# Kernel optimization log

Hardware: AMD Instinct MI355X
Metric: run time of the kernel (lower is better)

Reference implementation:

```python
import jax, jax.numpy as jnp
import numpy as np

ATOM_F = 64
NBR_F = 41
EPS = 1e-05


def setup_inputs() -> dict:
    key = jax.random.key(0)
    ks = jax.random.split(key, 10)
    B, N, M = 512, 64, 12
    F, NF = ATOM_F, NBR_F
    atom_fea = jax.random.normal(ks[0], (B, N, F), dtype=jnp.float32)
    nbr_fea = jax.random.normal(ks[1], (B, N, M, NF), dtype=jnp.float32)
    nbr_fea_idx = jax.random.randint(ks[2], (B, N, M), 0, N, dtype=jnp.int32)
    mask = jax.random.randint(ks[3], (B, N, M, 2 * F), 0, 2, dtype=jnp.int32)
    lim = float(np.sqrt(6.0 / (2 * F + NF + 2 * F)))
    gc_W = jax.random.uniform(ks[4], (2 * F + NF, 2 * F), minval=-lim, maxval=lim, dtype=jnp.float32)
    gc_bias = jnp.zeros((2 * F,), jnp.float32)
    gamma_1 = jnp.ones((2 * F,), jnp.float32)
    beta_1 = jnp.zeros((2 * F,), jnp.float32)
    gamma_2 = jnp.ones((F,), jnp.float32)
    beta_2 = jnp.zeros((F,), jnp.float32)
    return {
        'atom_fea': atom_fea, 'nbr_fea': nbr_fea, 'gc_W': gc_W, 'gc_bias': gc_bias,
        'gamma_1': gamma_1, 'beta_1': beta_1, 'gamma_2': gamma_2, 'beta_2': beta_2,
        'nbr_fea_idx': nbr_fea_idx, 'mask': mask,
    }


def _bn(x, mu, var, gamma, beta):
    return (x - mu) * jax.lax.rsqrt(var + EPS) * gamma + beta


def reference(atom_fea, nbr_fea, gc_W, gc_bias, gamma_1, beta_1, gamma_2, beta_2, nbr_fea_idx, mask):
    B, N, M = nbr_fea_idx.shape
    F = atom_fea.shape[-1]
    m = mask.astype(jnp.float32)                       # [B,N,M,2F]
    # gather neighbor atom features per batch: [B,N,M,F]
    atom_nbr_fea = jax.vmap(lambda af, idx: af[idx])(atom_fea, nbr_fea_idx)
    atom_exp = jnp.broadcast_to(atom_fea[:, :, None, :], (B, N, M, F))
    total_nbr_fea = jnp.concatenate([atom_exp, atom_nbr_fea, nbr_fea], axis=3)
    total_gated = (jnp.einsum('bnmk,ko->bnmo', total_nbr_fea, gc_W) + gc_bias) * m
    # global masked batchnorm (scalar mu/var over all nonzero entries)
    cnt1 = jnp.count_nonzero(total_gated).astype(jnp.float32)
    mu_1 = jnp.sum(total_gated) / cnt1
    var_1 = jnp.sum((total_gated - mu_1) ** 2 * m) / cnt1
    total_gated = _bn(total_gated, mu_1, var_1, gamma_1, beta_1) * m
    nbr_filter, nbr_core = jnp.split(total_gated, 2, axis=3)
    gated = jax.nn.sigmoid(nbr_filter) * jax.nn.softplus(nbr_core)
    m_node = m[:, :, 0, :F]                            # [B,N,F]
    nbr_summed = jnp.sum(gated, axis=2) * m_node
    cnt2 = jnp.count_nonzero(nbr_summed).astype(jnp.float32)
    mu_2 = jnp.sum(nbr_summed) / cnt2
    diff2 = (nbr_summed - mu_2) ** 2 * m_node
    var_2 = jnp.sum(diff2) / jnp.count_nonzero(diff2).astype(jnp.float32)
    nbr_summed = _bn(nbr_summed, mu_2, var_2, gamma_2, beta_2) * m_node
    return jax.nn.softplus(atom_fea + nbr_summed) * m_node
```

## Files before the change

kernel.cpp:

```cpp
#include <hip/hip_runtime.h>
#include <hip/hip_bf16.h>

#define B_   512
#define N_   64
#define M_   12
#define F_   64
#define NF_  41
#define NODES (B_*N_)
#define ROWS  (NODES*M_)
#define GW    NODES
#define GBLK  (GW/4)
#define ABLK  1024
#define KTOT  169
#define CSTR  136

typedef __bf16 bf16x8 __attribute__((ext_vector_type(8)));
typedef float  f32x4  __attribute__((ext_vector_type(4)));
typedef float  f32x4u __attribute__((ext_vector_type(4), aligned(4)));

#define P1_OFF 1024
#define P2_OFF 525312
#define WF_OFF 537600
#define X_OFF  586752

__device__ __forceinline__ float waveReduce(float v) {
#pragma unroll
  for (int off = 32; off > 0; off >>= 1) v += __shfl_down(v, off, 64);
  return v;
}

__device__ __forceinline__ bf16x8 cvt8(f32x4 a, f32x4 b) {
  bf16x8 r;
  r[0] = (__bf16)a[0]; r[1] = (__bf16)a[1]; r[2] = (__bf16)a[2]; r[3] = (__bf16)a[3];
  r[4] = (__bf16)b[0]; r[5] = (__bf16)b[1]; r[6] = (__bf16)b[2]; r[7] = (__bf16)b[3];
  return r;
}

__global__ void k_wprep(const float* __restrict__ W, __bf16* __restrict__ Wf) {
  int t = blockIdx.x * 256 + threadIdx.x;
  if (t >= 6 * 8 * 64) return;
  int lane = t & 63, nt = (t >> 6) & 7, kc = t >> 9;
  int n  = nt * 16 + (lane & 15);
  int k0 = kc * 32 + (lane >> 4) * 8;
  bf16x8 v;
#pragma unroll
  for (int j = 0; j < 8; j++) {
    int k = k0 + j;
    v[j] = (k < KTOT) ? (__bf16)W[k * 128 + n] : (__bf16)0.f;
  }
  *reinterpret_cast<bf16x8*>(&Wf[(size_t)t * 8]) = v;
}

__global__ __launch_bounds__(256, 4) void k_gemm(
    const float* __restrict__ atom, const float* __restrict__ nbr,
    const int* __restrict__ idx, const int* __restrict__ mask,
    const __bf16* __restrict__ Wf, const float* __restrict__ bias,
    float* __restrict__ part1, __bf16* __restrict__ xout)
{
  __shared__ __bf16 Cs_all[4][12 * CSTR];

  const int tid  = threadIdx.x;
  const int w    = tid >> 6;
  const int lane = tid & 63;
  const int nlo  = lane & 15;
  const int quad = lane >> 4;
  const int g    = blockIdx.x * 4 + w;
  const int bb   = (g >> 6) << 6;
  __bf16* Cs = Cs_all[w];

  const int r  = (nlo < 11) ? nlo : 11;
  const int nb = idx[g * M_ + r];

  bf16x8 af[6];
  {
    const float* p = &atom[(size_t)g * F_ + quad * 8];
    f32x4 a0 = *(const f32x4*)p, b0 = *(const f32x4*)(p + 4);
    f32x4 a1 = *(const f32x4*)(p + 32), b1 = *(const f32x4*)(p + 36);
    af[0] = cvt8(a0, b0); af[1] = cvt8(a1, b1);
  }
  {
    const float* p = &atom[(size_t)(bb + nb) * F_ + quad * 8];
    f32x4 a0 = *(const f32x4*)p, b0 = *(const f32x4*)(p + 4);
    f32x4 a1 = *(const f32x4*)(p + 32), b1 = *(const f32x4*)(p + 36);
    af[2] = cvt8(a0, b0); af[3] = cvt8(a1, b1);
  }
  {
    const float* nrow = &nbr[(size_t)(g * M_ + r) * NF_];
    f32x4u a0 = *(const f32x4u*)(nrow + quad * 8);
    f32x4u b0 = *(const f32x4u*)(nrow + quad * 8 + 4);
    af[4] = cvt8((f32x4)a0, (f32x4)b0);
    float t[8];
#pragma unroll
    for (int j = 0; j < 8; j++) {
      int kp = 32 + quad * 8 + j;
      t[j] = (kp < NF_) ? nrow[kp] : 0.f;
    }
    bf16x8 v;
#pragma unroll
    for (int j = 0; j < 8; j++) v[j] = (__bf16)t[j];
    af[5] = v;
  }

  f32x4 acc[8];
#pragma unroll
  for (int nt = 0; nt < 8; nt++) acc[nt] = (f32x4){0.f, 0.f, 0.f, 0.f};

#pragma unroll
  for (int kc = 0; kc < 6; kc++) {
#pragma unroll
    for (int nt = 0; nt < 8; nt++) {
      bf16x8 bf = *reinterpret_cast<const bf16x8*>(
          &Wf[(size_t)(((kc * 8 + nt) * 64) + lane) * 8]);
      acc[nt] = __builtin_amdgcn_mfma_f32_16x16x32_bf16(af[kc], bf, acc[nt], 0, 0, 0);
    }
  }

  if (quad < 3) {
#pragma unroll
    for (int nt = 0; nt < 8; nt++) {
      float bv = bias[nt * 16 + nlo];
#pragma unroll
      for (int reg = 0; reg < 4; reg++) {
        int row = quad * 4 + reg;
        Cs[row * CSTR + nt * 16 + nlo] = (__bf16)(acc[nt][reg] + bv);
      }
    }
  }
  asm volatile("s_waitcnt lgkmcnt(0)" ::: "memory");

  float s = 0.f, ss = 0.f, cz = 0.f, cm = 0.f;
#pragma unroll
  for (int i = 0; i < 3; i++) {
    int ch = lane + i * 64;
    int row = ch >> 4, c = ch & 15;
    size_t grow = (size_t)g * M_ + row;
    bf16x8 yv = *reinterpret_cast<const bf16x8*>(&Cs[row * CSTR + c * 8]);
    const int4 mA = *(const int4*)&mask[grow * 128 + c * 8];
    const int4 mB = *(const int4*)&mask[grow * 128 + c * 8 + 4];
    int mv[8] = {mA.x, mA.y, mA.z, mA.w, mB.x, mB.y, mB.z, mB.w};
#pragma unroll
    for (int j = 0; j < 8; j++) {
      float y = (float)yv[j];
      if (!mv[j]) { y = 0.f; yv[j] = (__bf16)0.f; }
      s += y; ss += y * y;
      cz += (y != 0.f) ? 1.f : 0.f;
      cm += (float)mv[j];
    }
    *reinterpret_cast<bf16x8*>(&xout[grow * 128 + c * 8]) = yv;
  }

  float v0 = waveReduce(s), v1 = waveReduce(ss), v2 = waveReduce(cz), v3 = waveReduce(cm);
  if (lane == 0) {
    part1[0 * GW + g] = v0;
    part1[1 * GW + g] = v1;
    part1[2 * GW + g] = v2;
    part1[3 * GW + g] = v3;
  }
}

__global__ __launch_bounds__(256) void k_red1(const float* __restrict__ part1,
                                              float* __restrict__ scal) {
  __shared__ double red[256][4];
  int t = threadIdx.x;
  double a[4] = {0.0, 0.0, 0.0, 0.0};
  for (int i = t; i < GW; i += 256)
#pragma unroll
    for (int q = 0; q < 4; q++) a[q] += (double)part1[q * GW + i];
#pragma unroll
  for (int q = 0; q < 4; q++) red[t][q] = a[q];
  __syncthreads();
  for (int s = 128; s > 0; s >>= 1) {
    if (t < s)
#pragma unroll
      for (int q = 0; q < 4; q++) red[t][q] += red[t + s][q];
    __syncthreads();
  }
  if (t == 0) {
    double S = red[0][0], SS = red[0][1], CNZ = red[0][2], CM = red[0][3];
    double mu = 0.0, var = 0.0;
    if (CNZ > 0.5) {
      mu = S / CNZ;
      var = (SS - 2.0 * mu * S + mu * mu * CM) / CNZ;
    }
    scal[0] = (float)mu;
    scal[1] = (float)(1.0 / sqrt(var + 1e-5));
  }
}

__global__ __launch_bounds__(256) void k_act(
    const __bf16* __restrict__ x, const int* __restrict__ mask,
    const float* __restrict__ g1, const float* __restrict__ b1,
    const float* __restrict__ scal, float* __restrict__ part2,
    float* __restrict__ ns)
{
  __shared__ float red[3][4];
  int t = blockIdx.x * 256 + threadIdx.x;
  int g = t >> 3, o0 = (t & 7) * 8;

  float mu1 = scal[0], inv1 = scal[1];

  float kf[8], cf[8], kc[8], cc[8];
#pragma unroll
  for (int j = 0; j < 8; j++) {
    kf[j] = inv1 * g1[o0 + j];      cf[j] = b1[o0 + j]      - mu1 * kf[j];
    kc[j] = inv1 * g1[64 + o0 + j]; cc[j] = b1[64 + o0 + j] - mu1 * kc[j];
  }

  size_t base = (size_t)g * (M_ * 128) + o0;
  float ssum[8];
#pragma unroll
  for (int j = 0; j < 8; j++) ssum[j] = 0.f;

#pragma unroll
  for (int m = 0; m < M_; m++) {
    bf16x8 xf = *reinterpret_cast<const bf16x8*>(&x[base + m * 128]);
    bf16x8 xc = *reinterpret_cast<const bf16x8*>(&x[base + m * 128 + 64]);
#pragma unroll
    for (int j = 0; j < 8; j++) {
      float vf = (float)xf[j], vc = (float)xc[j];
      float yf = (vf != 0.f) ? fmaf(vf, kf[j], cf[j]) : 0.f;
      float yc = (vc != 0.f) ? fmaf(vc, kc[j], cc[j]) : 0.f;
      float sg = __builtin_amdgcn_rcpf(1.f + __expf(-yf));
      float sp = fmaxf(yc, 0.f) + __logf(1.f + __expf(-fabsf(yc)));
      ssum[j] += sg * sp;
    }
  }

  const int4 mA = *(const int4*)&mask[(size_t)g * (M_ * 128) + o0];
  const int4 mB = *(const int4*)&mask[(size_t)g * (M_ * 128) + o0 + 4];
  int mn[8] = {mA.x, mA.y, mA.z, mA.w, mB.x, mB.y, mB.z, mB.w};
  float s = 0.f, ss2 = 0.f, c = 0.f;
  float v[8];
#pragma unroll
  for (int j = 0; j < 8; j++) {
    v[j] = mn[j] ? ssum[j] : 0.f;
    s += v[j]; ss2 += v[j] * v[j];
    c += (v[j] != 0.f) ? 1.f : 0.f;
  }
  *(float4*)&ns[(size_t)g * 64 + o0]     = (float4){v[0], v[1], v[2], v[3]};
  *(float4*)&ns[(size_t)g * 64 + o0 + 4] = (float4){v[4], v[5], v[6], v[7]};

  float v0 = waveReduce(s), v1 = waveReduce(ss2), v2 = waveReduce(c);
  int lane = threadIdx.x & 63, wid = threadIdx.x >> 6;
  if (lane == 0) { red[0][wid] = v0; red[1][wid] = v1; red[2][wid] = v2; }
  __syncthreads();
  if (threadIdx.x < 3)
    part2[threadIdx.x * ABLK + blockIdx.x] =
        red[threadIdx.x][0] + red[threadIdx.x][1] + red[threadIdx.x][2] + red[threadIdx.x][3];
}

__global__ __launch_bounds__(256) void k_red2(const float* __restrict__ part2,
                                              float* __restrict__ scal) {
  __shared__ double red[256][3];
  int t = threadIdx.x;
  double a[3] = {0.0, 0.0, 0.0};
  for (int i = t; i < ABLK; i += 256)
#pragma unroll
    for (int q = 0; q < 3; q++) a[q] += (double)part2[q * ABLK + i];
#pragma unroll
  for (int q = 0; q < 3; q++) red[t][q] = a[q];
  __syncthreads();
  for (int s = 128; s > 0; s >>= 1) {
    if (t < s)
#pragma unroll
      for (int q = 0; q < 3; q++) red[t][q] += red[t + s][q];
    __syncthreads();
  }
  if (t == 0) {
    double S = red[0][0], SS = red[0][1], C = red[0][2];
    double mu = 0.0, var = 0.0;
    if (C > 0.5) {
      mu = S / C;
      var = (SS - 2.0 * mu * S + mu * mu * C) / C;
    }
    scal[2] = (float)mu;
    scal[3] = (float)(1.0 / sqrt(var + 1e-5));
  }
}

__global__ __launch_bounds__(256) void k_out(
    const float* __restrict__ atom, const float* __restrict__ ns,
    const float* __restrict__ g2, const float* __restrict__ b2,
    const float* __restrict__ scal, float* __restrict__ out)
{
  int t = blockIdx.x * 256 + threadIdx.x;
  int g = t >> 3, o0 = (t & 7) * 8;
  float mu2 = scal[2], inv2 = scal[3];

  float4 n0 = *(const float4*)&ns[(size_t)g * 64 + o0];
  float4 n1 = *(const float4*)&ns[(size_t)g * 64 + o0 + 4];
  float4 a0 = *(const float4*)&atom[(size_t)g * 64 + o0];
  float4 a1 = *(const float4*)&atom[(size_t)g * 64 + o0 + 4];
  float nv[8] = {n0.x, n0.y, n0.z, n0.w, n1.x, n1.y, n1.z, n1.w};
  float av[8] = {a0.x, a0.y, a0.z, a0.w, a1.x, a1.y, a1.z, a1.w};
  float r[8];
#pragma unroll
  for (int j = 0; j < 8; j++) {
    r[j] = 0.f;
    if (nv[j] != 0.f) {
      float bn = (nv[j] - mu2) * inv2 * g2[o0 + j] + b2[o0 + j];
      float a = av[j] + bn;
      r[j] = fmaxf(a, 0.f) + __logf(1.f + __expf(-fabsf(a)));
    }
  }
  *(float4*)&out[(size_t)g * 64 + o0]     = (float4){r[0], r[1], r[2], r[3]};
  *(float4*)&out[(size_t)g * 64 + o0 + 4] = (float4){r[4], r[5], r[6], r[7]};
}

extern "C" void kernel_launch(void* const* d_in, const int* in_sizes, int n_in,
                              void* d_out, int out_size, void* d_ws, size_t ws_size,
                              hipStream_t stream)
{
  const float* atom = (const float*)d_in[0];
  const float* nbr  = (const float*)d_in[1];
  const float* W    = (const float*)d_in[2];
  const float* bias = (const float*)d_in[3];
  const float* g1   = (const float*)d_in[4];
  const float* b1   = (const float*)d_in[5];
  const float* g2   = (const float*)d_in[6];
  const float* b2   = (const float*)d_in[7];
  const int*   idx  = (const int*)d_in[8];
  const int*   mask = (const int*)d_in[9];
  float* out = (float*)d_out;

  char* ws = (char*)d_ws;
  float*  scal  = (float*)ws;
  float*  part1 = (float*)(ws + P1_OFF);
  float*  part2 = (float*)(ws + P2_OFF);
  __bf16* Wf    = (__bf16*)(ws + WF_OFF);
  __bf16* x     = (__bf16*)(ws + X_OFF);
  float* ns = out;

  k_wprep<<<12, 256, 0, stream>>>(W, Wf);
  k_gemm<<<GBLK, 256, 0, stream>>>(atom, nbr, idx, mask, Wf, bias, part1, x);
  k_red1<<<1, 256, 0, stream>>>(part1, scal);
  k_act<<<(NODES * 8) / 256, 256, 0, stream>>>(x, mask, g1, b1, scal, part2, ns);
  k_red2<<<1, 256, 0, stream>>>(part2, scal);
  k_out<<<(NODES * 8) / 256, 256, 0, stream>>>(atom, ns, g2, b2, scal, out);
}
```

Measured before the change: 480.2 us.

## Retile gather-GEMM so waves split output columns and keep weights in registers

The GEMM kernel used to give each wave one node (12 rows, padded to 16) and all 128 output columns, reloading the full weight fragment set per wave. Now each block handles 4 nodes (48 rows, exactly three 16-row MFMA tiles) per iteration and loops over 8 groups. Each wave owns 32 output columns, so its weight fragments are loaded into registers once and reused across iterations. This removes the 25% padding waste and the repeated weight loads, but cuts block count by 8x, lowers the occupancy hint, and makes every wave redundantly gather the same A operands.

```diff
diff --git a/kernel.cpp b/kernel.cpp
--- a/kernel.cpp
+++ b/kernel.cpp
@@ -8,20 +8,22 @@
 #define NF_  41
 #define NODES (B_*N_)
 #define ROWS  (NODES*M_)
-#define GW    NODES
-#define GBLK  (GW/4)
+#define GRP   (NODES/4)
+#define ITER  8
+#define BLKS  (GRP/ITER)
+#define WSLOT (BLKS*4)
 #define ABLK  1024
 #define KTOT  169
-#define CSTR  136
+#define CSTR2 40
 
 typedef __bf16 bf16x8 __attribute__((ext_vector_type(8)));
 typedef float  f32x4  __attribute__((ext_vector_type(4)));
 typedef float  f32x4u __attribute__((ext_vector_type(4), aligned(4)));
 
 #define P1_OFF 1024
-#define P2_OFF 525312
-#define WF_OFF 537600
-#define X_OFF  586752
+#define P2_OFF 66560
+#define WF_OFF 78848
+#define X_OFF  128000
 
 __device__ __forceinline__ float waveReduce(float v) {
 #pragma unroll
@@ -51,110 +53,133 @@
   *reinterpret_cast<bf16x8*>(&Wf[(size_t)t * 8]) = v;
 }
 
-__global__ __launch_bounds__(256, 4) void k_gemm(
+__global__ __launch_bounds__(256, 3) void k_gemm(
     const float* __restrict__ atom, const float* __restrict__ nbr,
     const int* __restrict__ idx, const int* __restrict__ mask,
     const __bf16* __restrict__ Wf, const float* __restrict__ bias,
     float* __restrict__ part1, __bf16* __restrict__ xout)
 {
-  __shared__ __bf16 Cs_all[4][12 * CSTR];
+  __shared__ __bf16 Cs_all[4][48 * CSTR2];
 
   const int tid  = threadIdx.x;
   const int w    = tid >> 6;
   const int lane = tid & 63;
   const int nlo  = lane & 15;
   const int quad = lane >> 4;
-  const int g    = blockIdx.x * 4 + w;
-  const int bb   = (g >> 6) << 6;
   __bf16* Cs = Cs_all[w];
 
-  const int r  = (nlo < 11) ? nlo : 11;
-  const int nb = idx[g * M_ + r];
-
-  bf16x8 af[6];
-  {
-    const float* p = &atom[(size_t)g * F_ + quad * 8];
-    f32x4 a0 = *(const f32x4*)p, b0 = *(const f32x4*)(p + 4);
-    f32x4 a1 = *(const f32x4*)(p + 32), b1 = *(const f32x4*)(p + 36);
-    af[0] = cvt8(a0, b0); af[1] = cvt8(a1, b1);
-  }
-  {
-    const float* p = &atom[(size_t)(bb + nb) * F_ + quad * 8];
-    f32x4 a0 = *(const f32x4*)p, b0 = *(const f32x4*)(p + 4);
-    f32x4 a1 = *(const f32x4*)(p + 32), b1 = *(const f32x4*)(p + 36);
-    af[2] = cvt8(a0, b0); af[3] = cvt8(a1, b1);
-  }
-  {
-    const float* nrow = &nbr[(size_t)(g * M_ + r) * NF_];
-    f32x4u a0 = *(const f32x4u*)(nrow + quad * 8);
-    f32x4u b0 = *(const f32x4u*)(nrow + quad * 8 + 4);
-    af[4] = cvt8((f32x4)a0, (f32x4)b0);
-    float t[8];
-#pragma unroll
-    for (int j = 0; j < 8; j++) {
-      int kp = 32 + quad * 8 + j;
-      t[j] = (kp < NF_) ? nrow[kp] : 0.f;
-    }
-    bf16x8 v;
-#pragma unroll
-    for (int j = 0; j < 8; j++) v[j] = (__bf16)t[j];
-    af[5] = v;
-  }
-
-  f32x4 acc[8];
-#pragma unroll
-  for (int nt = 0; nt < 8; nt++) acc[nt] = (f32x4){0.f, 0.f, 0.f, 0.f};
-
-#pragma unroll
-  for (int kc = 0; kc < 6; kc++) {
-#pragma unroll
-    for (int nt = 0; nt < 8; nt++) {
-      bf16x8 bf = *reinterpret_cast<const bf16x8*>(
-          &Wf[(size_t)(((kc * 8 + nt) * 64) + lane) * 8]);
-      acc[nt] = __builtin_amdgcn_mfma_f32_16x16x32_bf16(af[kc], bf, acc[nt], 0, 0, 0);
-    }
-  }
-
-  if (quad < 3) {
-#pragma unroll
-    for (int nt = 0; nt < 8; nt++) {
-      float bv = bias[nt * 16 + nlo];
-#pragma unroll
-      for (int reg = 0; reg < 4; reg++) {
-        int row = quad * 4 + reg;
-        Cs[row * CSTR + nt * 16 + nlo] = (__bf16)(acc[nt][reg] + bv);
+  bf16x8 Wreg[6][2];
+#pragma unroll
+  for (int kc = 0; kc < 6; kc++)
+#pragma unroll
+    for (int j = 0; j < 2; j++)
+      Wreg[kc][j] = *reinterpret_cast<const bf16x8*>(
+          &Wf[(size_t)(((kc * 8 + 2 * w + j) * 64) + lane) * 8]);
+
+  float bv[2];
+#pragma unroll
+  for (int j = 0; j < 2; j++) bv[j] = bias[(2 * w + j) * 16 + nlo];
+
+  float s = 0.f, ss = 0.f, cz = 0.f, cm = 0.f;
+
+  for (int it = 0; it < ITER; it++) {
+    const int grp = blockIdx.x * ITER + it;
+    const int g0  = grp * 4;
+    const int bb  = (g0 >> 6) << 6;
+    const size_t row0 = (size_t)g0 * M_;
+
+    f32x4 acc[3][2];
+#pragma unroll
+    for (int mt = 0; mt < 3; mt++)
+#pragma unroll
+      for (int j = 0; j < 2; j++) acc[mt][j] = (f32x4){0.f, 0.f, 0.f, 0.f};
+
+#pragma unroll
+    for (int mt = 0; mt < 3; mt++) {
+      const int row  = mt * 16 + nlo;
+      const int node = row / 12;
+      const int nb   = idx[row0 + row];
+
+      const float* pa = &atom[(size_t)(g0 + node) * F_ + quad * 8];
+      f32x4 a0 = *(const f32x4*)pa,        a1 = *(const f32x4*)(pa + 4);
+      f32x4 a2 = *(const f32x4*)(pa + 32), a3 = *(const f32x4*)(pa + 36);
+
+      const float* pg = &atom[(size_t)(bb + nb) * F_ + quad * 8];
+      f32x4 g0v = *(const f32x4*)pg,        g1v = *(const f32x4*)(pg + 4);
+      f32x4 g2v = *(const f32x4*)(pg + 32), g3v = *(const f32x4*)(pg + 36);
+
+      const float* nrow = &nbr[(row0 + row) * NF_];
+      f32x4 n0 = (f32x4)*(const f32x4u*)(nrow + quad * 8);
+      f32x4 n1 = (f32x4)*(const f32x4u*)(nrow + quad * 8 + 4);
+
+      bf16x8 af0 = cvt8(a0, a1), af1 = cvt8(a2, a3);
+      bf16x8 af2 = cvt8(g0v, g1v), af3 = cvt8(g2v, g3v);
+      bf16x8 af4 = cvt8(n0, n1);
+      bf16x8 af5;
+#pragma unroll
+      for (int j = 0; j < 8; j++) af5[j] = (__bf16)0.f;
+      if (quad == 0) {
+        f32x4 t0 = (f32x4)*(const f32x4u*)(nrow + 32);
+        f32x4 t1 = (f32x4)*(const f32x4u*)(nrow + 36);
+        af5 = cvt8(t0, t1);
+      } else if (quad == 1) {
+        af5[0] = (__bf16)nrow[40];
       }
-    }
-  }
-  asm volatile("s_waitcnt lgkmcnt(0)" ::: "memory");
-
-  float s = 0.f, ss = 0.f, cz = 0.f, cm = 0.f;
-#pragma unroll
-  for (int i = 0; i < 3; i++) {
-    int ch = lane + i * 64;
-    int row = ch >> 4, c = ch & 15;
-    size_t grow = (size_t)g * M_ + row;
-    bf16x8 yv = *reinterpret_cast<const bf16x8*>(&Cs[row * CSTR + c * 8]);
-    const int4 mA = *(const int4*)&mask[grow * 128 + c * 8];
-    const int4 mB = *(const int4*)&mask[grow * 128 + c * 8 + 4];
-    int mv[8] = {mA.x, mA.y, mA.z, mA.w, mB.x, mB.y, mB.z, mB.w};
-#pragma unroll
-    for (int j = 0; j < 8; j++) {
-      float y = (float)yv[j];
-      if (!mv[j]) { y = 0.f; yv[j] = (__bf16)0.f; }
-      s += y; ss += y * y;
-      cz += (y != 0.f) ? 1.f : 0.f;
-      cm += (float)mv[j];
-    }
-    *reinterpret_cast<bf16x8*>(&xout[grow * 128 + c * 8]) = yv;
+
+      acc[mt][0] = __builtin_amdgcn_mfma_f32_16x16x32_bf16(af0, Wreg[0][0], acc[mt][0], 0, 0, 0);
+      acc[mt][1] = __builtin_amdgcn_mfma_f32_16x16x32_bf16(af0, Wreg[0][1], acc[mt][1], 0, 0, 0);
+      acc[mt][0] = __builtin_amdgcn_mfma_f32_16x16x32_bf16(af1, Wreg[1][0], acc[mt][0], 0, 0, 0);
+      acc[mt][1] = __builtin_amdgcn_mfma_f32_16x16x32_bf16(af1, Wreg[1][1], acc[mt][1], 0, 0, 0);
+      acc[mt][0] = __builtin_amdgcn_mfma_f32_16x16x32_bf16(af2, Wreg[2][0], acc[mt][0], 0, 0, 0);
+      acc[mt][1] = __builtin_amdgcn_mfma_f32_16x16x32_bf16(af2, Wreg[2][1], acc[mt][1], 0, 0, 0);
+      acc[mt][0] = __builtin_amdgcn_mfma_f32_16x16x32_bf16(af3, Wreg[3][0], acc[mt][0], 0, 0, 0);
+      acc[mt][1] = __builtin_amdgcn_mfma_f32_16x16x32_bf16(af3, Wreg[3][1], acc[mt][1], 0, 0, 0);
+      acc[mt][0] = __builtin_amdgcn_mfma_f32_16x16x32_bf16(af4, Wreg[4][0], acc[mt][0], 0, 0, 0);
+      acc[mt][1] = __builtin_amdgcn_mfma_f32_16x16x32_bf16(af4, Wreg[4][1], acc[mt][1], 0, 0, 0);
+      acc[mt][0] = __builtin_amdgcn_mfma_f32_16x16x32_bf16(af5, Wreg[5][0], acc[mt][0], 0, 0, 0);
+      acc[mt][1] = __builtin_amdgcn_mfma_f32_16x16x32_bf16(af5, Wreg[5][1], acc[mt][1], 0, 0, 0);
+    }
+
+#pragma unroll
+    for (int mt = 0; mt < 3; mt++)
+#pragma unroll
+      for (int reg = 0; reg < 4; reg++)
+#pragma unroll
+        for (int j = 0; j < 2; j++) {
+          int row = mt * 16 + quad * 4 + reg;
+          Cs[row * CSTR2 + j * 16 + nlo] = (__bf16)(acc[mt][j][reg] + bv[j]);
+        }
+    asm volatile("s_waitcnt lgkmcnt(0)" ::: "memory");
+
+#pragma unroll
+    for (int i = 0; i < 3; i++) {
+      int ch  = lane + i * 64;
+      int row = ch >> 2, c = ch & 3;
+      size_t grow = row0 + row;
+      size_t gcol = (size_t)grow * 128 + w * 32 + c * 8;
+      bf16x8 yv = *reinterpret_cast<const bf16x8*>(&Cs[row * CSTR2 + c * 8]);
+      const int4 mA = *(const int4*)&mask[gcol];
+      const int4 mB = *(const int4*)&mask[gcol + 4];
+      int mv[8] = {mA.x, mA.y, mA.z, mA.w, mB.x, mB.y, mB.z, mB.w};
+#pragma unroll
+      for (int j = 0; j < 8; j++) {
+        float y = (float)yv[j];
+        if (!mv[j]) { y = 0.f; yv[j] = (__bf16)0.f; }
+        s += y; ss += y * y;
+        cz += (y != 0.f) ? 1.f : 0.f;
+        cm += (float)mv[j];
+      }
+      *reinterpret_cast<bf16x8*>(&xout[gcol]) = yv;
+    }
   }
 
   float v0 = waveReduce(s), v1 = waveReduce(ss), v2 = waveReduce(cz), v3 = waveReduce(cm);
   if (lane == 0) {
-    part1[0 * GW + g] = v0;
-    part1[1 * GW + g] = v1;
-    part1[2 * GW + g] = v2;
-    part1[3 * GW + g] = v3;
+    int slot = blockIdx.x * 4 + w;
+    part1[0 * WSLOT + slot] = v0;
+    part1[1 * WSLOT + slot] = v1;
+    part1[2 * WSLOT + slot] = v2;
+    part1[3 * WSLOT + slot] = v3;
   }
 }
 
@@ -163,9 +188,9 @@
   __shared__ double red[256][4];
   int t = threadIdx.x;
   double a[4] = {0.0, 0.0, 0.0, 0.0};
-  for (int i = t; i < GW; i += 256)
-#pragma unroll
-    for (int q = 0; q < 4; q++) a[q] += (double)part1[q * GW + i];
+  for (int i = t; i < WSLOT; i += 256)
+#pragma unroll
+    for (int q = 0; q < 4; q++) a[q] += (double)part1[q * WSLOT + i];
 #pragma unroll
   for (int q = 0; q < 4; q++) red[t][q] = a[q];
   __syncthreads();
@@ -332,7 +357,7 @@
   float* ns = out;
 
   k_wprep<<<12, 256, 0, stream>>>(W, Wf);
-  k_gemm<<<GBLK, 256, 0, stream>>>(atom, nbr, idx, mask, Wf, bias, part1, x);
+  k_gemm<<<BLKS, 256, 0, stream>>>(atom, nbr, idx, mask, Wf, bias, part1, x);
   k_red1<<<1, 256, 0, stream>>>(part1, scal);
   k_act<<<(NODES * 8) / 256, 256, 0, stream>>>(x, mask, g1, b1, scal, part2, ns);
   k_red2<<<1, 256, 0, stream>>>(part2, scal);
```

Measured after the change: 474.2 us. Within noise of the previous version (-1.2%).
